# Performance work log

Hardware: AMD Instinct MI355X
Metric: run time of the kernel (lower is better)

## Reference

```python
import jax, jax.numpy as jnp
import numpy as np

N_NODES = 100_000
N_EDGES = 1_600_000
N_GRAPHS = 1_000
VOCAB = 65
D_IN = 128
D_HID = 128


def setup_inputs() -> dict:
    key = jax.random.key(0)
    ks = jax.random.split(key, 12)
    x = jax.random.randint(ks[0], (N_NODES,), 0, VOCAB)
    edge_index = jax.random.randint(ks[1], (2, N_EDGES), 0, N_NODES)
    batch = jnp.sort(jax.random.randint(ks[2], (N_NODES,), 0, N_GRAPHS))

    def lin(k, fan_in, fan_out):
        bound = 1.0 / np.sqrt(fan_in)
        kw, kb = jax.random.split(k)
        W = jax.random.uniform(kw, (fan_in, fan_out), jnp.float32, -bound, bound)
        b = jax.random.uniform(kb, (fan_out,), jnp.float32, -bound, bound)
        return W, b

    emb = jax.random.normal(ks[3], (VOCAB, D_IN), jnp.float32)
    W1, b1 = lin(ks[4], D_IN, D_HID)
    W2, b2 = lin(ks[5], D_HID, D_HID)
    W3, b3 = lin(ks[6], D_HID, D_HID)
    Wf, bf = lin(ks[7], D_HID, 1)
    return {"x": x, "edge_index": edge_index, "batch": batch, "emb": emb,
            "W1": W1, "b1": b1, "W2": W2, "b2": b2, "W3": W3, "b3": b3,
            "Wf": Wf, "bf": bf}


def gcn_conv(h, W, b, src, dst, n):
    # PyG GCNConv: add self-loops, symmetric normalization D^-1/2 A_hat D^-1/2,
    # transform then aggregate messages at dst.
    h = h @ W                                             # [N, H]
    deg = jnp.zeros((n,), h.dtype).at[dst].add(1.0) + 1.0  # self-loop adds 1
    dinv = jax.lax.rsqrt(deg)                             # [N]
    coef = dinv[src] * dinv[dst]                          # [E]
    agg = jax.ops.segment_sum(h[src] * coef[:, None], dst, num_segments=n)
    return agg + h * (dinv * dinv)[:, None] + b           # self-loop term + bias


def reference(x, edge_index, batch, emb, W1, b1, W2, b2, W3, b3, Wf, bf):
    # Embedding with max_norm=1: renormalize looked-up rows to norm <= 1.
    e = emb[x]                                            # [N, D_IN]
    nrm = jnp.linalg.norm(e, axis=-1, keepdims=True)
    e = e * jnp.minimum(1.0, 1.0 / jnp.maximum(nrm, 1e-7))

    src, dst = edge_index[0], edge_index[1]
    h = jax.nn.relu(gcn_conv(e, W1, b1, src, dst, N_NODES))
    h = jax.nn.relu(gcn_conv(h, W2, b2, src, dst, N_NODES))
    h = jax.nn.relu(gcn_conv(h, W3, b3, src, dst, N_NODES))

    g = jax.ops.segment_max(h, batch, num_segments=N_GRAPHS)  # [G, H]
    return (g @ Wf + bf).ravel()                               # [G]
```

## Files before the change

kernel.cpp:

```cpp
#include <hip/hip_runtime.h>
#include <hip/hip_bf16.h>

#define N_NODES  100000
#define N_EDGES  1600000
#define N_GRAPHS 1000
#define D        128
#define CAP      64
#define NBKT     256
#define N_BUCKETS ((N_NODES + NBKT - 1) / NBKT)
#define HWGS     256
#define EPW      ((N_EDGES + HWGS - 1) / HWGS)

typedef __attribute__((ext_vector_type(8))) short bf16x8;
typedef __attribute__((ext_vector_type(4))) float f32x4;

__device__ inline f32x4 mfma16(bf16x8 a, bf16x8 b, f32x4 c) {
    return __builtin_amdgcn_mfma_f32_16x16x32_bf16(a, b, c, 0, 0, 0);
}

__device__ inline unsigned short f2bf(float f) {
    unsigned u = __float_as_uint(f);
    unsigned r = u + 0x7fffu + ((u >> 16) & 1u);
    return (unsigned short)(r >> 16);
}

__global__ __launch_bounds__(256) void k_hist(const int* __restrict__ dst,
                                              int* __restrict__ bcnt,
                                              int* __restrict__ wgoff) {
    __shared__ int hist[N_BUCKETS];
    int t = threadIdx.x, w = blockIdx.x;
    for (int b = t; b < N_BUCKETS; b += 256) hist[b] = 0;
    __syncthreads();
    int e0 = w * EPW, e1 = min(e0 + EPW, N_EDGES);
    for (int i = e0 + t; i < e1; i += 256)
        atomicAdd(&hist[dst[i] >> 8], 1);
    __syncthreads();
    for (int b = t; b < N_BUCKETS; b += 256) {
        int h = hist[b];
        wgoff[w * N_BUCKETS + b] = h ? atomicAdd(&bcnt[b], h) : 0;
    }
}

__global__ __launch_bounds__(512) void k_bscan(const int* __restrict__ bcnt,
                                               int* __restrict__ boff) {
    __shared__ int s[512];
    int t = threadIdx.x;
    int v = (t < N_BUCKETS) ? bcnt[t] : 0;
    s[t] = v;
    __syncthreads();
    for (int off = 1; off < 512; off <<= 1) {
        int val = (t >= off) ? s[t - off] : 0;
        __syncthreads();
        s[t] += val;
        __syncthreads();
    }
    if (t < N_BUCKETS) boff[t] = s[t] - v;
    if (t == 0) boff[N_BUCKETS] = N_EDGES;
}

__global__ __launch_bounds__(256) void k_scat(const int* __restrict__ src,
                                              const int* __restrict__ dst,
                                              const int* __restrict__ boff,
                                              const int* __restrict__ wgoff,
                                              int2* __restrict__ epair) {
    __shared__ int cnt[N_BUCKETS];
    int t = threadIdx.x, w = blockIdx.x;
    for (int b = t; b < N_BUCKETS; b += 256) cnt[b] = 0;
    __syncthreads();
    int e0 = w * EPW, e1 = min(e0 + EPW, N_EDGES);
    for (int i = e0 + t; i < e1; i += 256) {
        int d = dst[i], b = d >> 8;
        int r = atomicAdd(&cnt[b], 1);
        epair[boff[b] + wgoff[w * N_BUCKETS + b] + r] = make_int2(src[i], d);
    }
}

__global__ __launch_bounds__(256) void k_ell(const int2* __restrict__ epair,
                                             const int* __restrict__ boff,
                                             int* __restrict__ ell,
                                             int* __restrict__ fill) {
    __shared__ int cnt_s[NBKT];
    __shared__ int ell_s[NBKT * CAP];
    int t = threadIdx.x, b = blockIdx.x;
    int nb0 = b * NBKT;
    int nn = min(NBKT, N_NODES - nb0);
    for (int i = t; i < NBKT; i += 256) cnt_s[i] = 0;
    __syncthreads();
    int e0 = boff[b], e1 = boff[b + 1];
    for (int i = e0 + t; i < e1; i += 256) {
        int2 e = epair[i];
        int ln = e.y - nb0;
        int r = atomicAdd(&cnt_s[ln], 1);
        if (r < CAP) ell_s[ln * CAP + r] = e.x;
    }
    __syncthreads();
    for (int i = t; i < nn * CAP; i += 256)
        ell[(size_t)nb0 * CAP + i] = ell_s[i];
    if (t < nn) fill[nb0 + t] = cnt_s[t];
}

__global__ __launch_bounds__(256) void k_embed(const int* __restrict__ x,
                                               const float* __restrict__ emb,
                                               unsigned short* __restrict__ h) {
    int n = blockIdx.x * 4 + (threadIdx.x >> 6);
    int lane = threadIdx.x & 63;
    if (n >= N_NODES) return;
    int xi = x[n];
    float2 v = ((const float2*)(emb + (size_t)xi * D))[lane];
    float ss = v.x * v.x + v.y * v.y;
    #pragma unroll
    for (int off = 32; off; off >>= 1) ss += __shfl_xor(ss, off);
    float nrm = sqrtf(ss);
    float scale = fminf(1.0f, 1.0f / fmaxf(nrm, 1e-7f));
    unsigned pk = (unsigned)f2bf(v.x * scale) | ((unsigned)f2bf(v.y * scale) << 16);
    ((unsigned*)(h + (size_t)n * D))[lane] = pk;
}

__global__ __launch_bounds__(256) void k_gemm(const unsigned short* __restrict__ A,
                                              const float* __restrict__ W,
                                              const int* __restrict__ fill,
                                              unsigned short* __restrict__ Cb) {
    __shared__ short Bh[2048 * 8];
    __shared__ short Bl[2048 * 8];
    int t = threadIdx.x;
    #pragma unroll
    for (int f = 0; f < 8; f++) {
        int id = t + f * 256;
        int lane = id & 63, kb = (id >> 6) & 3, nt = id >> 8;
        int k0 = kb * 32 + (lane >> 4) * 8;
        int n  = nt * 16 + (lane & 15);
        bf16x8 vh, vl;
        #pragma unroll
        for (int j = 0; j < 8; j++) {
            float wv = W[(k0 + j) * 128 + n];
            unsigned short hs = f2bf(wv);
            float hf = __uint_as_float((unsigned)hs << 16);
            vh[j] = (short)hs;
            vl[j] = (short)f2bf(wv - hf);
        }
        *(bf16x8*)&Bh[id * 8] = vh;
        *(bf16x8*)&Bl[id * 8] = vl;
    }
    __syncthreads();

    int w = t >> 6, lane = t & 63;
    int quad = lane >> 4, col = lane & 15;
    size_t r0 = (size_t)blockIdx.x * 128 + w * 32;
    f32x4 acc[2][8];
    #pragma unroll
    for (int r = 0; r < 2; r++)
        #pragma unroll
        for (int n = 0; n < 8; n++) acc[r][n] = (f32x4){0.f, 0.f, 0.f, 0.f};

    #pragma unroll
    for (int kb = 0; kb < 4; kb++) {
        bf16x8 a0 = *(const bf16x8*)&A[(r0 + col)      * D + kb * 32 + quad * 8];
        bf16x8 a1 = *(const bf16x8*)&A[(r0 + 16 + col) * D + kb * 32 + quad * 8];
        #pragma unroll
        for (int nt = 0; nt < 8; nt++) {
            bf16x8 bh = *(const bf16x8*)&Bh[((nt * 4 + kb) * 64 + lane) * 8];
            bf16x8 bl = *(const bf16x8*)&Bl[((nt * 4 + kb) * 64 + lane) * 8];
            acc[0][nt] = mfma16(a0, bh, acc[0][nt]);
            acc[0][nt] = mfma16(a0, bl, acc[0][nt]);
            acc[1][nt] = mfma16(a1, bh, acc[1][nt]);
            acc[1][nt] = mfma16(a1, bl, acc[1][nt]);
        }
    }
    #pragma unroll
    for (int r = 0; r < 2; r++) {
        size_t row = r0 + r * 16 + quad * 4;
        #pragma unroll
        for (int g = 0; g < 4; g++) {
            float dv = (row + g < N_NODES)
                         ? 1.0f / sqrtf((float)fill[row + g] + 1.0f) : 0.f;
            #pragma unroll
            for (int nt = 0; nt < 8; nt++)
                Cb[(row + g) * D + nt * 16 + col] = f2bf(acc[r][nt][g] * dv);
        }
    }
}

__device__ inline void acc8m(float* acc, int4 r, float m) {
    unsigned u0 = (unsigned)r.x, u1 = (unsigned)r.y,
             u2 = (unsigned)r.z, u3 = (unsigned)r.w;
    acc[0] += __uint_as_float(u0 << 16) * m;
    acc[1] += __uint_as_float(u0 & 0xffff0000u) * m;
    acc[2] += __uint_as_float(u1 << 16) * m;
    acc[3] += __uint_as_float(u1 & 0xffff0000u) * m;
    acc[4] += __uint_as_float(u2 << 16) * m;
    acc[5] += __uint_as_float(u2 & 0xffff0000u) * m;
    acc[6] += __uint_as_float(u3 << 16) * m;
    acc[7] += __uint_as_float(u3 & 0xffff0000u) * m;
}

template<int BF16OUT>
__global__ __launch_bounds__(256) void k_agg(const unsigned short* __restrict__ hw2,
                                             void* __restrict__ hout,
                                             const int* __restrict__ fill,
                                             const int* __restrict__ ell,
                                             const float* __restrict__ bias) {
    int n = blockIdx.x * 4 + (threadIdx.x >> 6);
    int lane = threadIdx.x & 63;
    if (n >= N_NODES) return;
    int quad = lane >> 4;
    int l16  = lane & 15;
    int fr   = __builtin_amdgcn_readfirstlane(fill[n]);
    int cnt  = min(fr, CAP);

    float acc[8];
    #pragma unroll
    for (int c = 0; c < 8; c++) acc[c] = 0.f;

    int s_l = (lane < cnt) ? ell[(size_t)n * CAP + lane] : 0;
    for (int j = 0; j < cnt; j += 16) {
        int s0 = __shfl(s_l, j + quad);
        int s1 = __shfl(s_l, j + 4  + quad);
        int s2 = __shfl(s_l, j + 8  + quad);
        int s3 = __shfl(s_l, j + 12 + quad);
        float m0 = (j + quad      < cnt) ? 1.f : 0.f;
        float m1 = (j + 4  + quad < cnt) ? 1.f : 0.f;
        float m2 = (j + 8  + quad < cnt) ? 1.f : 0.f;
        float m3 = (j + 12 + quad < cnt) ? 1.f : 0.f;
        int4 r0 = *(const int4*)&hw2[(size_t)s0 * D + l16 * 8];
        int4 r1 = *(const int4*)&hw2[(size_t)s1 * D + l16 * 8];
        int4 r2 = *(const int4*)&hw2[(size_t)s2 * D + l16 * 8];
        int4 r3 = *(const int4*)&hw2[(size_t)s3 * D + l16 * 8];
        acc8m(acc, r0, m0);
        acc8m(acc, r1, m1);
        acc8m(acc, r2, m2);
        acc8m(acc, r3, m3);
    }
    #pragma unroll
    for (int c = 0; c < 8; c++) {
        acc[c] += __shfl_xor(acc[c], 16);
        acc[c] += __shfl_xor(acc[c], 32);
    }
    if (quad == 0) {
        int4 sr = *(const int4*)&hw2[(size_t)n * D + l16 * 8];
        acc8m(acc, sr, 1.f);
        float di = 1.0f / sqrtf((float)fr + 1.0f);
        float4 bA = *(const float4*)&bias[l16 * 8];
        float4 bB = *(const float4*)&bias[l16 * 8 + 4];
        float o[8];
        o[0] = fmaxf(acc[0] * di + bA.x, 0.f);
        o[1] = fmaxf(acc[1] * di + bA.y, 0.f);
        o[2] = fmaxf(acc[2] * di + bA.z, 0.f);
        o[3] = fmaxf(acc[3] * di + bA.w, 0.f);
        o[4] = fmaxf(acc[4] * di + bB.x, 0.f);
        o[5] = fmaxf(acc[5] * di + bB.y, 0.f);
        o[6] = fmaxf(acc[6] * di + bB.z, 0.f);
        o[7] = fmaxf(acc[7] * di + bB.w, 0.f);
        if (BF16OUT) {
            int4 pk;
            pk.x = (int)((unsigned)f2bf(o[0]) | ((unsigned)f2bf(o[1]) << 16));
            pk.y = (int)((unsigned)f2bf(o[2]) | ((unsigned)f2bf(o[3]) << 16));
            pk.z = (int)((unsigned)f2bf(o[4]) | ((unsigned)f2bf(o[5]) << 16));
            pk.w = (int)((unsigned)f2bf(o[6]) | ((unsigned)f2bf(o[7]) << 16));
            *(int4*)&((unsigned short*)hout)[(size_t)n * D + l16 * 8] = pk;
        } else {
            float* orow = (float*)hout + (size_t)n * D + l16 * 8;
            *(float4*)orow       = make_float4(o[0], o[1], o[2], o[3]);
            *(float4*)(orow + 4) = make_float4(o[4], o[5], o[6], o[7]);
        }
    }
}

__global__ void k_bounds(const int* __restrict__ batch, int* __restrict__ gstart,
                         int* __restrict__ gend) {
    int i = blockIdx.x * 256 + threadIdx.x;
    if (i < N_NODES) {
        int b = batch[i];
        atomicMin(&gstart[b], i);
        atomicMax(&gend[b], i + 1);
    }
}

__global__ __launch_bounds__(256) void k_pool(const float* __restrict__ h,
                                              const int* __restrict__ gstart,
                                              const int* __restrict__ gend,
                                              const float* __restrict__ Wf,
                                              const float* __restrict__ bf,
                                              float* __restrict__ out) {
    __shared__ float2 sm[4][64];
    int g = blockIdx.x;
    int w = threadIdx.x >> 6, lane = threadIdx.x & 63;
    int s = gstart[g], e = gend[g];
    float2 m = make_float2(-3.402823466e38f, -3.402823466e38f);
    for (int i = s + w; i < e; i += 4) {
        float2 v = ((const float2*)(h + (size_t)i * D))[lane];
        m.x = fmaxf(m.x, v.x);
        m.y = fmaxf(m.y, v.y);
    }
    sm[w][lane] = m;
    __syncthreads();
    if (w == 0) {
        float2 a = sm[0][lane], b2 = sm[1][lane], c = sm[2][lane], d = sm[3][lane];
        m.x = fmaxf(fmaxf(a.x, b2.x), fmaxf(c.x, d.x));
        m.y = fmaxf(fmaxf(a.y, b2.y), fmaxf(c.y, d.y));
        float2 wf = ((const float2*)Wf)[lane];
        float val = m.x * wf.x + m.y * wf.y;
        #pragma unroll
        for (int off = 32; off; off >>= 1) val += __shfl_xor(val, off);
        if (lane == 0) out[g] = val + bf[0];
    }
}

extern "C" void kernel_launch(void* const* d_in, const int* in_sizes, int n_in,
                              void* d_out, int out_size, void* d_ws, size_t ws_size,
                              hipStream_t stream) {
    const int*   x    = (const int*)d_in[0];
    const int*   ei   = (const int*)d_in[1];
    const int*   batch= (const int*)d_in[2];
    const float* emb  = (const float*)d_in[3];
    const float* W1   = (const float*)d_in[4];
    const float* b1   = (const float*)d_in[5];
    const float* W2   = (const float*)d_in[6];
    const float* b2   = (const float*)d_in[7];
    const float* W3   = (const float*)d_in[8];
    const float* b3   = (const float*)d_in[9];
    const float* Wf   = (const float*)d_in[10];
    const float* bf   = (const float*)d_in[11];
    float* out = (float*)d_out;

    const int* src = ei;
    const int* dst = ei + N_EDGES;

    char* p = (char*)d_ws;
    float*          hA   = (float*)p;          p += (size_t)(N_NODES + 128) * D * 4;
    unsigned short* hAb  = (unsigned short*)hA;
    unsigned short* hwb  = (unsigned short*)p; p += (size_t)(N_NODES + 128) * D * 2;
    int2*           epair= (int2*)hwb;
    int*   fill     = (int*)p;              p += (size_t)N_NODES * 4;
    int*   gend     = (int*)p;              p += (size_t)N_GRAPHS * 4;
    int*   gstart   = (int*)p;              p += (size_t)N_GRAPHS * 4;
    int*   ell      = (int*)p;              p += (size_t)N_NODES * CAP * 4;
    int*   wgoff    = (int*)p;              p += (size_t)HWGS * N_BUCKETS * 4;
    int*   bcnt     = (int*)p;              p += (size_t)(N_BUCKETS + 4) * 4;
    int*   boff     = (int*)p;              p += (size_t)(N_BUCKETS + 4) * 4;
    (void)p;

    hipMemsetAsync(bcnt, 0, (size_t)N_BUCKETS * 4, stream);
    hipMemsetAsync(gend, 0, (size_t)N_GRAPHS * 4, stream);
    hipMemsetAsync(gstart, 0x7f, (size_t)N_GRAPHS * 4, stream);

    const int NB = (N_NODES + 255) / 256;
    const int NW = (N_NODES + 3) / 4;
    const int GB = (N_NODES + 127) / 128;

    k_hist <<<HWGS, 256, 0, stream>>>(dst, bcnt, wgoff);
    k_bscan<<<1, 512, 0, stream>>>(bcnt, boff);
    k_scat <<<HWGS, 256, 0, stream>>>(src, dst, boff, wgoff, epair);
    k_ell  <<<N_BUCKETS, 256, 0, stream>>>(epair, boff, ell, fill);

    k_embed<<<NW, 256, 0, stream>>>(x, emb, hAb);

    k_gemm  <<<GB, 256, 0, stream>>>(hAb, W1, fill, hwb);
    k_agg<1><<<NW, 256, 0, stream>>>(hwb, hAb, fill, ell, b1);
    k_gemm  <<<GB, 256, 0, stream>>>(hAb, W2, fill, hwb);
    k_agg<1><<<NW, 256, 0, stream>>>(hwb, hAb, fill, ell, b2);
    k_gemm  <<<GB, 256, 0, stream>>>(hAb, W3, fill, hwb);
    k_agg<0><<<NW, 256, 0, stream>>>(hwb, hA, fill, ell, b3);

    k_bounds<<<NB, 256, 0, stream>>>(batch, gstart, gend);
    k_pool  <<<N_GRAPHS, 256, 0, stream>>>(hA, gstart, gend, Wf, bf, out);
}
```

Before: 454.5 us.

## Precompute split-bf16 weight fragments once and software-pipeline aggregation gathers

Adds a small kernel that converts W1..W3 into hi/lo bf16 MFMA fragments once, so each GEMM block copies prepared fragments into shared memory instead of reconverting fp32 weights per block. The aggregation loop drops the per-neighbor mask multiply by pointing padding lanes at a sentinel row (index N_NODES, assumed zeroed). It also double-buffers the gathered rows so the next set of loads is in flight while the current one is accumulated. The changes add register pressure and rely on the padding row being zero.

```diff
diff --git a/kernel.cpp b/kernel.cpp
--- a/kernel.cpp
+++ b/kernel.cpp
@@ -99,6 +99,35 @@
     if (t < nn) fill[nb0 + t] = cnt_s[t];
 }
 
+__global__ __launch_bounds__(256) void k_wprep(const float* __restrict__ W1,
+                                               const float* __restrict__ W2,
+                                               const float* __restrict__ W3,
+                                               short* __restrict__ frag) {
+    int L = blockIdx.x;
+    const float* W = (L == 0) ? W1 : (L == 1) ? W2 : W3;
+    short* fh = frag + (size_t)L * 32768;
+    short* fl = fh + 16384;
+    int t = threadIdx.x;
+    #pragma unroll
+    for (int f = 0; f < 8; f++) {
+        int id = t + f * 256;
+        int lane = id & 63, kb = (id >> 6) & 3, nt = id >> 8;
+        int k0 = kb * 32 + (lane >> 4) * 8;
+        int n  = nt * 16 + (lane & 15);
+        bf16x8 vh, vl;
+        #pragma unroll
+        for (int j = 0; j < 8; j++) {
+            float wv = W[(k0 + j) * 128 + n];
+            unsigned short hs = f2bf(wv);
+            float hf = __uint_as_float((unsigned)hs << 16);
+            vh[j] = (short)hs;
+            vl[j] = (short)f2bf(wv - hf);
+        }
+        *(bf16x8*)&fh[id * 8] = vh;
+        *(bf16x8*)&fl[id * 8] = vl;
+    }
+}
+
 __global__ __launch_bounds__(256) void k_embed(const int* __restrict__ x,
                                                const float* __restrict__ emb,
                                                unsigned short* __restrict__ h) {
@@ -117,31 +146,20 @@
 }
 
 __global__ __launch_bounds__(256) void k_gemm(const unsigned short* __restrict__ A,
-                                              const float* __restrict__ W,
+                                              const short* __restrict__ frag,
                                               const int* __restrict__ fill,
                                               unsigned short* __restrict__ Cb) {
-    __shared__ short Bh[2048 * 8];
-    __shared__ short Bl[2048 * 8];
+    __shared__ short Bfrag[2 * 16384];
     int t = threadIdx.x;
-    #pragma unroll
-    for (int f = 0; f < 8; f++) {
-        int id = t + f * 256;
-        int lane = id & 63, kb = (id >> 6) & 3, nt = id >> 8;
-        int k0 = kb * 32 + (lane >> 4) * 8;
-        int n  = nt * 16 + (lane & 15);
-        bf16x8 vh, vl;
-        #pragma unroll
-        for (int j = 0; j < 8; j++) {
-            float wv = W[(k0 + j) * 128 + n];
-            unsigned short hs = f2bf(wv);
-            float hf = __uint_as_float((unsigned)hs << 16);
-            vh[j] = (short)hs;
-            vl[j] = (short)f2bf(wv - hf);
-        }
-        *(bf16x8*)&Bh[id * 8] = vh;
-        *(bf16x8*)&Bl[id * 8] = vl;
-    }
-    __syncthreads();
+    {
+        const int4* g4 = (const int4*)frag;
+        int4* l4 = (int4*)Bfrag;
+        #pragma unroll
+        for (int i = 0; i < 16; i++) l4[t + i * 256] = g4[t + i * 256];
+    }
+    __syncthreads();
+    const short* Bh = Bfrag;
+    const short* Bl = Bfrag + 16384;
 
     int w = t >> 6, lane = t & 63;
     int quad = lane >> 4, col = lane & 15;
@@ -180,17 +198,17 @@
     }
 }
 
-__device__ inline void acc8m(float* acc, int4 r, float m) {
+__device__ inline void acc8(float* acc, int4 r) {
     unsigned u0 = (unsigned)r.x, u1 = (unsigned)r.y,
              u2 = (unsigned)r.z, u3 = (unsigned)r.w;
-    acc[0] += __uint_as_float(u0 << 16) * m;
-    acc[1] += __uint_as_float(u0 & 0xffff0000u) * m;
-    acc[2] += __uint_as_float(u1 << 16) * m;
-    acc[3] += __uint_as_float(u1 & 0xffff0000u) * m;
-    acc[4] += __uint_as_float(u2 << 16) * m;
-    acc[5] += __uint_as_float(u2 & 0xffff0000u) * m;
-    acc[6] += __uint_as_float(u3 << 16) * m;
-    acc[7] += __uint_as_float(u3 & 0xffff0000u) * m;
+    acc[0] += __uint_as_float(u0 << 16);
+    acc[1] += __uint_as_float(u0 & 0xffff0000u);
+    acc[2] += __uint_as_float(u1 << 16);
+    acc[3] += __uint_as_float(u1 & 0xffff0000u);
+    acc[4] += __uint_as_float(u2 << 16);
+    acc[5] += __uint_as_float(u2 & 0xffff0000u);
+    acc[6] += __uint_as_float(u3 << 16);
+    acc[7] += __uint_as_float(u3 & 0xffff0000u);
 }
 
 template<int BF16OUT>
@@ -204,6 +222,7 @@
     if (n >= N_NODES) return;
     int quad = lane >> 4;
     int l16  = lane & 15;
+    unsigned cOff = (unsigned)(l16 << 3);
     int fr   = __builtin_amdgcn_readfirstlane(fill[n]);
     int cnt  = min(fr, CAP);
 
@@ -211,33 +230,37 @@
     #pragma unroll
     for (int c = 0; c < 8; c++) acc[c] = 0.f;
 
-    int s_l = (lane < cnt) ? ell[(size_t)n * CAP + lane] : 0;
-    for (int j = 0; j < cnt; j += 16) {
-        int s0 = __shfl(s_l, j + quad);
-        int s1 = __shfl(s_l, j + 4  + quad);
-        int s2 = __shfl(s_l, j + 8  + quad);
-        int s3 = __shfl(s_l, j + 12 + quad);
-        float m0 = (j + quad      < cnt) ? 1.f : 0.f;
-        float m1 = (j + 4  + quad < cnt) ? 1.f : 0.f;
-        float m2 = (j + 8  + quad < cnt) ? 1.f : 0.f;
-        float m3 = (j + 12 + quad < cnt) ? 1.f : 0.f;
-        int4 r0 = *(const int4*)&hw2[(size_t)s0 * D + l16 * 8];
-        int4 r1 = *(const int4*)&hw2[(size_t)s1 * D + l16 * 8];
-        int4 r2 = *(const int4*)&hw2[(size_t)s2 * D + l16 * 8];
-        int4 r3 = *(const int4*)&hw2[(size_t)s3 * D + l16 * 8];
-        acc8m(acc, r0, m0);
-        acc8m(acc, r1, m1);
-        acc8m(acc, r2, m2);
-        acc8m(acc, r3, m3);
-    }
+    int s_l = (lane < cnt) ? ell[(size_t)n * CAP + lane] : N_NODES;
+
+    int iters = (cnt + 15) >> 4;
+    int4 Ra[4], Rb[4];
+    #pragma unroll
+    for (int k = 0; k < 4; k++) {
+        int s = __shfl(s_l, k * 4 + quad);
+        Ra[k] = *(const int4*)&hw2[((unsigned)s << 7) + cOff];
+    }
+    for (int it = 1; it < iters; it++) {
+        #pragma unroll
+        for (int k = 0; k < 4; k++) {
+            int s = __shfl(s_l, it * 16 + k * 4 + quad);
+            Rb[k] = *(const int4*)&hw2[((unsigned)s << 7) + cOff];
+        }
+        #pragma unroll
+        for (int k = 0; k < 4; k++) acc8(acc, Ra[k]);
+        #pragma unroll
+        for (int k = 0; k < 4; k++) Ra[k] = Rb[k];
+    }
+    #pragma unroll
+    for (int k = 0; k < 4; k++) acc8(acc, Ra[k]);
+
     #pragma unroll
     for (int c = 0; c < 8; c++) {
         acc[c] += __shfl_xor(acc[c], 16);
         acc[c] += __shfl_xor(acc[c], 32);
     }
     if (quad == 0) {
-        int4 sr = *(const int4*)&hw2[(size_t)n * D + l16 * 8];
-        acc8m(acc, sr, 1.f);
+        int4 sr = *(const int4*)&hw2[((unsigned)n << 7) + cOff];
+        acc8(acc, sr);
         float di = 1.0f / sqrtf((float)fr + 1.0f);
         float4 bA = *(const float4*)&bias[l16 * 8];
         float4 bB = *(const float4*)&bias[l16 * 8 + 4];
@@ -256,9 +279,9 @@
             pk.y = (int)((unsigned)f2bf(o[2]) | ((unsigned)f2bf(o[3]) << 16));
             pk.z = (int)((unsigned)f2bf(o[4]) | ((unsigned)f2bf(o[5]) << 16));
             pk.w = (int)((unsigned)f2bf(o[6]) | ((unsigned)f2bf(o[7]) << 16));
-            *(int4*)&((unsigned short*)hout)[(size_t)n * D + l16 * 8] = pk;
+            *(int4*)&((unsigned short*)hout)[((unsigned)n << 7) + cOff] = pk;
         } else {
-            float* orow = (float*)hout + (size_t)n * D + l16 * 8;
+            float* orow = (float*)hout + ((size_t)n << 7) + cOff;
             *(float4*)orow       = make_float4(o[0], o[1], o[2], o[3]);
             *(float4*)(orow + 4) = make_float4(o[4], o[5], o[6], o[7]);
         }
@@ -337,6 +360,7 @@
     int*   wgoff    = (int*)p;              p += (size_t)HWGS * N_BUCKETS * 4;
     int*   bcnt     = (int*)p;              p += (size_t)(N_BUCKETS + 4) * 4;
     int*   boff     = (int*)p;              p += (size_t)(N_BUCKETS + 4) * 4;
+    short* wfrag    = (short*)p;            p += (size_t)3 * 32768 * 2;
     (void)p;
 
     hipMemsetAsync(bcnt, 0, (size_t)N_BUCKETS * 4, stream);
@@ -352,13 +376,14 @@
     k_scat <<<HWGS, 256, 0, stream>>>(src, dst, boff, wgoff, epair);
     k_ell  <<<N_BUCKETS, 256, 0, stream>>>(epair, boff, ell, fill);
 
+    k_wprep<<<3, 256, 0, stream>>>(W1, W2, W3, wfrag);
     k_embed<<<NW, 256, 0, stream>>>(x, emb, hAb);
 
-    k_gemm  <<<GB, 256, 0, stream>>>(hAb, W1, fill, hwb);
+    k_gemm  <<<GB, 256, 0, stream>>>(hAb, wfrag,             fill, hwb);
     k_agg<1><<<NW, 256, 0, stream>>>(hwb, hAb, fill, ell, b1);
-    k_gemm  <<<GB, 256, 0, stream>>>(hAb, W2, fill, hwb);
+    k_gemm  <<<GB, 256, 0, stream>>>(hAb, wfrag + 32768,     fill, hwb);
     k_agg<1><<<NW, 256, 0, stream>>>(hwb, hAb, fill, ell, b2);
-    k_gemm  <<<GB, 256, 0, stream>>>(hAb, W3, fill, hwb);
+    k_gemm  <<<GB, 256, 0, stream>>>(hAb, wfrag + 65536,     fill, hwb);
     k_agg<0><<<NW, 256, 0, stream>>>(hwb, hA, fill, ell, b3);
 
     k_bounds<<<NB, 256, 0, stream>>>(batch, gstart, gend);
```

New measurement: 450.2 us. Within noise of the previous version (-0.9%).
